# Kernel optimization log

Measured on AMD Instinct MI355X. Metric: run time of the kernel, lower is better.

The kernel has to match this reference:

```python
import jax, jax.numpy as jnp
import numpy as np

N = 100000       # num nodes
E = 1000000      # num edges
D_IN = 128       # input feature dim
D_H = 64         # hidden = output dim
EPS = 1e-5       # GraphNorm eps
SLOPE = 0.2      # LeakyReLU negative slope


def _glorot(key, shape):
    lim = float(np.sqrt(6.0 / (shape[0] + shape[1])))
    return jax.random.uniform(key, shape, jnp.float32, -lim, lim)


def setup_inputs() -> dict:
    key = jax.random.key(0)
    ks = jax.random.split(key, 6)
    return {
        "x": jax.random.normal(ks[0], (N, D_IN), jnp.float32),
        "edge_index": jax.random.randint(ks[1], (2, E), 0, N),
        "W_in": _glorot(ks[2], (D_IN, D_H)),
        "b_in": jnp.zeros((D_H,), jnp.float32),
        "W1": _glorot(ks[3], (D_H, D_H)),
        "b1": jnp.zeros((D_H,), jnp.float32),
        "gn1_alpha": jnp.ones((D_H,), jnp.float32),
        "gn1_gamma": jnp.ones((D_H,), jnp.float32),
        "gn1_beta": jnp.zeros((D_H,), jnp.float32),
        "W2": _glorot(ks[4], (D_H, D_H)),
        "b2": jnp.zeros((D_H,), jnp.float32),
        "gn2_alpha": jnp.ones((D_H,), jnp.float32),
        "gn2_gamma": jnp.ones((D_H,), jnp.float32),
        "gn2_beta": jnp.zeros((D_H,), jnp.float32),
    }


def gcn_conv(x, W, b, src, dst):
    # GCNConv with added self-loops and symmetric normalization:
    # out = D^{-1/2} (A + I) D^{-1/2} (x W) + b
    xw = x @ W                                                 # [N, D]
    ones = jnp.ones((src.shape[0],), x.dtype)
    deg = jax.ops.segment_sum(ones, dst, num_segments=x.shape[0]) + 1.0  # +1 self-loop
    dinv = jax.lax.rsqrt(deg)                                  # [N]
    coef = dinv[src] * dinv[dst]                               # [E]
    agg = jax.ops.segment_sum(xw[src] * coef[:, None], dst, num_segments=x.shape[0])
    return agg + xw * (dinv * dinv)[:, None] + b


def graph_norm(x, alpha, gamma, beta):
    # PyG GraphNorm over a single graph: per-feature mean/var over all nodes
    mean = jnp.mean(x, axis=0)
    c = x - alpha * mean
    var = jnp.mean(c * c, axis=0)
    return gamma * c * jax.lax.rsqrt(var + EPS) + beta


def reference(x, edge_index, W_in, b_in, W1, b1, gn1_alpha, gn1_gamma, gn1_beta,
              W2, b2, gn2_alpha, gn2_gamma, gn2_beta):
    src, dst = edge_index[0], edge_index[1]
    h = x @ W_in + b_in                                        # input projection
    h = graph_norm(gcn_conv(h, W1, b1, src, dst), gn1_alpha, gn1_gamma, gn1_beta)
    h = jnp.where(h > 0, h, SLOPE * h)                         # LeakyReLU(0.2); dropout=eval (identity)
    h = graph_norm(gcn_conv(h, W2, b2, src, dst), gn2_alpha, gn2_gamma, gn2_beta)
    return h                                                    # [N, D_H]
```

## Files before the change

### kernel.cpp

```cpp
#include <hip/hip_runtime.h>
#include <stdint.h>

#define N_NODES 100000
#define N_EDGES 1000000
#define D_IN 128
#define D_H 64
#define EPS 1e-5f
#define SLOPE 0.2f

typedef unsigned short u16;
typedef unsigned int u32;

__device__ __forceinline__ float bf2f(u16 u) {
    union { u32 i; float f; } v; v.i = ((u32)u) << 16; return v.f;
}
__device__ __forceinline__ u16 f2bf(float f) {
    union { float f; u32 i; } v; v.f = f;
    u32 r = (v.i + 0x7fffu + ((v.i >> 16) & 1u)) >> 16;
    return (u16)r;
}
__device__ __forceinline__ bool is_f32(const void* flagp) {
    return *(const u32*)flagp == 0x3F800000u;
}
__device__ __forceinline__ float loadf(const void* p, size_t i, bool m) {
    return m ? ((const float*)p)[i] : bf2f(((const u16*)p)[i]);
}

__global__ void kprep(const void* __restrict__ W_in, const void* __restrict__ b_in,
                      const void* __restrict__ W1, const void* __restrict__ flagp,
                      float* __restrict__ Wc, float* __restrict__ bc)
{
    bool m = is_f32(flagp);
    int c = blockIdx.x;
    int t = threadIdx.x;
    __shared__ float w1c[D_H];
    if (t < D_H) w1c[t] = loadf(W1, t * D_H + c, m);
    __syncthreads();
    float acc = 0.f;
    #pragma unroll 8
    for (int j = 0; j < D_H; j++) acc += loadf(W_in, t * D_H + j, m) * w1c[j];
    Wc[t * D_H + c] = acc;
    if (t == 0) {
        float b = 0.f;
        for (int j = 0; j < D_H; j++) b += loadf(b_in, j, m) * w1c[j];
        bc[c] = b;
    }
}

__global__ void kfill(const int* __restrict__ ei, int* __restrict__ cnt,
                      int* __restrict__ bucket)
{
    int e = blockIdx.x * blockDim.x + threadIdx.x;
    if (e >= N_EDGES) return;
    int s = ei[e];
    int d = ei[N_EDGES + e];
    int slot = atomicAdd(&cnt[d], 1);
    if (slot < 64) bucket[(size_t)d * 64 + slot] = s;
}

__global__ void kdinv(const int* __restrict__ cnt, float* __restrict__ dinv,
                      u16* __restrict__ xwb_pad)
{
    int i = blockIdx.x * blockDim.x + threadIdx.x;
    if (i < D_H) xwb_pad[(size_t)N_NODES * D_H + i] = 0;
    if (i >= N_NODES) return;
    dinv[i] = rsqrtf((float)cnt[i] + 1.0f);
}

__global__ __launch_bounds__(256) void kgemm1(const void* __restrict__ x,
        const float* __restrict__ Wc, const float* __restrict__ bc,
        const float* __restrict__ dinv, const void* __restrict__ flagp,
        u16* __restrict__ xwb)
{
    bool m = is_f32(flagp);
    __shared__ __align__(16) u16 xs[64 * 132];
    __shared__ float WL[D_IN * D_H];
    int tid = threadIdx.x;
    int row0 = blockIdx.x * 64;
    for (int i = tid; i < D_IN * D_H / 4; i += 256)
        ((float4*)WL)[i] = ((const float4*)Wc)[i];
    for (int i = tid; i < 64 * 32; i += 256) {
        int r = i >> 5, kq = (i & 31) * 4;
        int gr = row0 + r;
        ushort4 u = make_ushort4(0, 0, 0, 0);
        if (gr < N_NODES) {
            if (m) {
                float4 v = *(const float4*)((const float*)x + (size_t)gr * D_IN + kq);
                u = make_ushort4(f2bf(v.x), f2bf(v.y), f2bf(v.z), f2bf(v.w));
            } else {
                u = *(const ushort4*)((const u16*)x + (size_t)gr * D_IN + kq);
            }
        }
        *(ushort4*)(xs + r * 132 + kq) = u;
    }
    __syncthreads();
    int tx = tid & 15, ry = tid >> 4;
    float4 bcv = ((const float4*)bc)[tx];
    float acc[4][4];
    #pragma unroll
    for (int j = 0; j < 4; j++) { acc[j][0] = bcv.x; acc[j][1] = bcv.y; acc[j][2] = bcv.z; acc[j][3] = bcv.w; }
    #pragma unroll 4
    for (int k = 0; k < D_IN; k += 2) {
        float4 w0 = *(const float4*)(WL + k * D_H + tx * 4);
        float4 w1 = *(const float4*)(WL + (k + 1) * D_H + tx * 4);
        #pragma unroll
        for (int j = 0; j < 4; j++) {
            u32 p = *(const u32*)(xs + (ry * 4 + j) * 132 + k);
            float xl = bf2f((u16)(p & 0xffffu));
            float xh = bf2f((u16)(p >> 16));
            acc[j][0] += xl * w0.x; acc[j][1] += xl * w0.y; acc[j][2] += xl * w0.z; acc[j][3] += xl * w0.w;
            acc[j][0] += xh * w1.x; acc[j][1] += xh * w1.y; acc[j][2] += xh * w1.z; acc[j][3] += xh * w1.w;
        }
    }
    #pragma unroll
    for (int j = 0; j < 4; j++) {
        int gr = row0 + ry * 4 + j;
        if (gr < N_NODES) {
            float ds = dinv[gr];
            *(ushort4*)(xwb + (size_t)gr * D_H + tx * 4) =
                make_ushort4(f2bf(acc[j][0] * ds), f2bf(acc[j][1] * ds),
                             f2bf(acc[j][2] * ds), f2bf(acc[j][3] * ds));
        }
    }
}

__global__ __launch_bounds__(256) void kagg(const u16* __restrict__ xwb,
        const float* __restrict__ dinv, const int* __restrict__ cnt,
        const int* __restrict__ bucket, const void* __restrict__ bvec,
        const void* __restrict__ flagp, u16* __restrict__ ybuf,
        float* __restrict__ accum)
{
    bool m = is_f32(flagp);
    __shared__ __align__(16) char smem[4][8192];
    __shared__ float red_s[4][64], red_q[4][64];
    int tid = threadIdx.x;
    int wv = tid >> 6, L = tid & 63;
    int half = L >> 5, mm = L & 31;
    int node0 = blockIdx.x * 32 + wv * 8;

    int cnt8 = cnt[node0 + (L & 7)];
    float di8 = dinv[node0 + (L & 7)];
    int deg[8]; float dd[8];
    #pragma unroll
    for (int t = 0; t < 8; t++) {
        deg[t] = min(__builtin_amdgcn_readlane(cnt8, t), 64);
        dd[t] = __uint_as_float(__builtin_amdgcn_readlane(__float_as_uint(di8), t));
    }
    float b0 = loadf(bvec, 2 * mm, m), b1 = loadf(bvec, 2 * mm + 1, m);

    float ls0 = 0, ls1 = 0, lq0 = 0, lq1 = 0;
    char* base = &smem[wv][0];

    #pragma unroll
    for (int b = 0; b < 2; b++) {
        int nb = node0 + b * 4;
        int tl = L >> 4, sl = L & 15;
        int i_l = nb + tl;
        int raw = bucket[(size_t)i_l * 64 + sl];
        int degL = min(__shfl(cnt8, b * 4 + tl), 64);
        int src = (sl < degL) ? raw : ((sl == degL) ? i_l : N_NODES);

        #pragma unroll
        for (int k = 0; k < 8; k++) {
            int srcK = __shfl(src, k * 8 + (L >> 3));
            const u16* gp = xwb + (size_t)srcK * D_H + (L & 7) * 8;
            __builtin_amdgcn_global_load_lds(gp, base + k * 1024, 16, 0, 0);
        }
        __builtin_amdgcn_s_waitcnt(0);
        __builtin_amdgcn_sched_barrier(0);
        asm volatile("" ::: "memory");

        float A0 = 0, A1 = 0, C0 = 0, C1 = 0;
        #pragma unroll
        for (int p = 0; p < 2; p++) {
            int np = p * 2 + half;
            const u32* rp = (const u32*)(base + np * 2048);
            float a0 = 0, a1 = 0;
            #pragma unroll
            for (int s = 0; s < 16; s++) {
                u32 v = rp[s * 32 + mm];
                a0 += __uint_as_float(v << 16);
                a1 += __uint_as_float(v & 0xffff0000u);
            }
            if (p == 0) { A0 = a0; A1 = a1; } else { C0 = a0; C1 = a1; }
        }
        #pragma unroll
        for (int t = 0; t < 4; t++) {
            int degt = deg[b * 4 + t];
            if (degt >= 16) {
                int i = nb + t;
                float r0 = 0, r1 = 0;
                for (int s = 16 + half; s <= degt; s += 2) {
                    int sv = (s < degt) ? bucket[(size_t)i * 64 + s] : i;
                    u32 v = *((const u32*)(xwb + (size_t)sv * D_H) + mm);
                    r0 += __uint_as_float(v << 16);
                    r1 += __uint_as_float(v & 0xffff0000u);
                }
                r0 += __shfl_xor(r0, 32);
                r1 += __shfl_xor(r1, 32);
                bool mine = (half == (t & 1));
                if (t < 2) { A0 += mine ? r0 : 0.f; A1 += mine ? r1 : 0.f; }
                else       { C0 += mine ? r0 : 0.f; C1 += mine ? r1 : 0.f; }
            }
        }
        #pragma unroll
        for (int p = 0; p < 2; p++) {
            float a0 = p ? C0 : A0, a1 = p ? C1 : A1;
            float ddv = half ? dd[b * 4 + p * 2 + 1] : dd[b * 4 + p * 2];
            float y0 = ddv * a0 + b0;
            float y1 = ddv * a1 + b1;
            int node = nb + p * 2 + half;
            ((u32*)(ybuf + (size_t)node * D_H))[mm] =
                (u32)f2bf(y0) | ((u32)f2bf(y1) << 16);
            ls0 += y0; ls1 += y1; lq0 += y0 * y0; lq1 += y1 * y1;
        }
        asm volatile("" ::: "memory");
    }

    ls0 += __shfl_xor(ls0, 32); ls1 += __shfl_xor(ls1, 32);
    lq0 += __shfl_xor(lq0, 32); lq1 += __shfl_xor(lq1, 32);
    if (half == 0) {
        *(float2*)&red_s[wv][2 * mm] = make_float2(ls0, ls1);
        *(float2*)&red_q[wv][2 * mm] = make_float2(lq0, lq1);
    }
    __syncthreads();
    if (tid < 64) {
        atomicAdd(&accum[tid],      red_s[0][tid] + red_s[1][tid] + red_s[2][tid] + red_s[3][tid]);
        atomicAdd(&accum[64 + tid], red_q[0][tid] + red_q[1][tid] + red_q[2][tid] + red_q[3][tid]);
    }
}

__global__ void kparams(const float* __restrict__ accum, const void* __restrict__ alpha,
        const void* __restrict__ gamma, const void* __restrict__ beta,
        const void* __restrict__ flagp, float* __restrict__ params)
{
    bool m = is_f32(flagp);
    int f = threadIdx.x;
    float mean = accum[f] * (1.0f / N_NODES);
    float al = loadf(alpha, f, m);
    float var = accum[64 + f] * (1.0f / N_NODES) - mean * mean * al * (2.0f - al);
    var = fmaxf(var, 0.f);
    float a = loadf(gamma, f, m) * rsqrtf(var + EPS);
    params[f] = a;
    params[64 + f] = loadf(beta, f, m) - a * al * mean;
}

__global__ __launch_bounds__(256) void kgemm2(const u16* __restrict__ y1b,
        const void* __restrict__ W2, const float* __restrict__ params,
        const float* __restrict__ dinv, const void* __restrict__ flagp,
        u16* __restrict__ xwb)
{
    bool m = is_f32(flagp);
    __shared__ __align__(16) u16 hs[64 * 68];
    __shared__ float WL[D_H * D_H];
    __shared__ float aL[64], cL[64];
    int tid = threadIdx.x;
    if (tid < 64) { aL[tid] = params[tid]; cL[tid] = params[64 + tid]; }
    for (int i = tid; i < D_H * D_H; i += 256) WL[i] = loadf(W2, i, m);
    __syncthreads();
    int row0 = blockIdx.x * 64;
    for (int i = tid; i < 64 * 16; i += 256) {
        int r = i >> 4, kq = (i & 15) * 4;
        int gr = row0 + r;
        ushort4 u = make_ushort4(0, 0, 0, 0);
        if (gr < N_NODES) u = *(const ushort4*)(y1b + (size_t)gr * D_H + kq);
        float h0 = aL[kq + 0] * bf2f(u.x) + cL[kq + 0]; h0 = h0 > 0.f ? h0 : SLOPE * h0;
        float h1 = aL[kq + 1] * bf2f(u.y) + cL[kq + 1]; h1 = h1 > 0.f ? h1 : SLOPE * h1;
        float h2 = aL[kq + 2] * bf2f(u.z) + cL[kq + 2]; h2 = h2 > 0.f ? h2 : SLOPE * h2;
        float h3 = aL[kq + 3] * bf2f(u.w) + cL[kq + 3]; h3 = h3 > 0.f ? h3 : SLOPE * h3;
        *(ushort4*)(hs + r * 68 + kq) = make_ushort4(f2bf(h0), f2bf(h1), f2bf(h2), f2bf(h3));
    }
    __syncthreads();
    int tx = tid & 15, ry = tid >> 4;
    float acc[4][4] = {};
    #pragma unroll 4
    for (int k = 0; k < D_H; k += 2) {
        float4 w0 = *(const float4*)(WL + k * D_H + tx * 4);
        float4 w1 = *(const float4*)(WL + (k + 1) * D_H + tx * 4);
        #pragma unroll
        for (int j = 0; j < 4; j++) {
            u32 p = *(const u32*)(hs + (ry * 4 + j) * 68 + k);
            float xl = bf2f((u16)(p & 0xffffu));
            float xh = bf2f((u16)(p >> 16));
            acc[j][0] += xl * w0.x; acc[j][1] += xl * w0.y; acc[j][2] += xl * w0.z; acc[j][3] += xl * w0.w;
            acc[j][0] += xh * w1.x; acc[j][1] += xh * w1.y; acc[j][2] += xh * w1.z; acc[j][3] += xh * w1.w;
        }
    }
    #pragma unroll
    for (int j = 0; j < 4; j++) {
        int gr = row0 + ry * 4 + j;
        if (gr < N_NODES) {
            float ds = dinv[gr];
            *(ushort4*)(xwb + (size_t)gr * D_H + tx * 4) =
                make_ushort4(f2bf(acc[j][0] * ds), f2bf(acc[j][1] * ds),
                             f2bf(acc[j][2] * ds), f2bf(acc[j][3] * ds));
        }
    }
}

__global__ void kout(const u16* __restrict__ y2b, const float* __restrict__ params2,
                     const void* __restrict__ flagp, void* __restrict__ out)
{
    bool m = is_f32(flagp);
    int idx = blockIdx.x * blockDim.x + threadIdx.x;
    if (idx >= N_NODES * D_H) return;
    int f = idx & 63;
    float v = params2[f] * bf2f(y2b[idx]) + params2[64 + f];
    if (m) ((float*)out)[idx] = v;
    else   ((u16*)out)[idx] = f2bf(v);
}

extern "C" void kernel_launch(void* const* d_in, const int* in_sizes, int n_in,
                              void* d_out, int out_size, void* d_ws, size_t ws_size,
                              hipStream_t stream)
{
    const void* x    = d_in[0];
    const int*  ei   = (const int*)d_in[1];
    const void* W_in = d_in[2];
    const void* b_in = d_in[3];
    const void* W1   = d_in[4];
    const void* b1   = d_in[5];
    const void* gn1a = d_in[6];
    const void* gn1g = d_in[7];
    const void* gn1b = d_in[8];
    const void* W2   = d_in[9];
    const void* b2   = d_in[10];
    const void* gn2a = d_in[11];
    const void* gn2g = d_in[12];
    const void* gn2b = d_in[13];

    char* ws = (char*)d_ws;
    int*   cnt    = (int*)(ws + 0);
    float* accum  = (float*)(ws + 400000);
    float* params = (float*)(ws + 401024);
    float* bc     = (float*)(ws + 402048);
    float* Wc     = (float*)(ws + 402432);
    float* dinv   = (float*)(ws + 435200);
    int*   bucket = (int*)(ws + 1235200);
    u16*   bufA   = (u16*)(ws + 26835200);
    u16*   bufB   = (u16*)(ws + 39635456);

    hipMemsetAsync(ws, 0, 400000 + 1024, stream);

    kprep<<<64, 128, 0, stream>>>(W_in, b_in, W1, gn1a, Wc, bc);
    kfill<<<(N_EDGES + 255) / 256, 256, 0, stream>>>(ei, cnt, bucket);
    kdinv<<<(N_NODES + 255) / 256, 256, 0, stream>>>(cnt, dinv, bufA);
    kgemm1<<<(N_NODES + 63) / 64, 256, 0, stream>>>(x, Wc, bc, dinv, gn1a, bufA);
    kagg<<<N_NODES / 32, 256, 0, stream>>>(bufA, dinv, cnt, bucket, b1, gn1a, bufB, accum);
    kparams<<<1, 64, 0, stream>>>(accum, gn1a, gn1g, gn1b, gn1a, params);
    kgemm2<<<(N_NODES + 63) / 64, 256, 0, stream>>>(bufB, W2, params, dinv, gn1a, bufA);
    kagg<<<N_NODES / 32, 256, 0, stream>>>(bufA, dinv, cnt, bucket, b2, gn1a, bufB, accum + 128);
    kparams<<<1, 64, 0, stream>>>(accum + 128, gn2a, gn2g, gn2b, gn1a, params + 128);
    kout<<<(N_NODES * D_H + 255) / 256, 256, 0, stream>>>(bufB, params + 128, gn1a, d_out);
}
```

Before: 434.5 us.

## Use bf16 MFMA instructions for both dense projection GEMMs

Replaces the scalar FP32 FMA inner loops in kgemm1 and kgemm2 with 16x16x32 bf16 MFMA instructions. The combined input weight and W2 are now pre-transposed and stored as bf16 by kprep, so each wave can load its B fragments contiguously from padded LDS. The aim is to cut the ALU cost of the two dense matmuls. In exchange the weights are rounded to bf16, and output stores shrink from ushort4 to scattered 2-byte writes.

```diff
diff --git a/kernel.cpp b/kernel.cpp
--- a/kernel.cpp
+++ b/kernel.cpp
@@ -1,5 +1,6 @@
 #include <hip/hip_runtime.h>
 #include <stdint.h>
+#include <string.h>
 
 #define N_NODES 100000
 #define N_EDGES 1000000
@@ -10,6 +11,8 @@
 
 typedef unsigned short u16;
 typedef unsigned int u32;
+typedef __attribute__((ext_vector_type(8))) short bf16x8;
+typedef __attribute__((ext_vector_type(4))) float f32x4;
 
 __device__ __forceinline__ float bf2f(u16 u) {
     union { u32 i; float f; } v; v.i = ((u32)u) << 16; return v.f;
@@ -27,23 +30,31 @@
 }
 
 __global__ void kprep(const void* __restrict__ W_in, const void* __restrict__ b_in,
-                      const void* __restrict__ W1, const void* __restrict__ flagp,
-                      float* __restrict__ Wc, float* __restrict__ bc)
-{
-    bool m = is_f32(flagp);
-    int c = blockIdx.x;
+                      const void* __restrict__ W1, const void* __restrict__ W2,
+                      const void* __restrict__ flagp,
+                      u16* __restrict__ WcT, u16* __restrict__ W2T,
+                      float* __restrict__ bc)
+{
+    bool m = is_f32(flagp);
     int t = threadIdx.x;
-    __shared__ float w1c[D_H];
-    if (t < D_H) w1c[t] = loadf(W1, t * D_H + c, m);
-    __syncthreads();
-    float acc = 0.f;
-    #pragma unroll 8
-    for (int j = 0; j < D_H; j++) acc += loadf(W_in, t * D_H + j, m) * w1c[j];
-    Wc[t * D_H + c] = acc;
-    if (t == 0) {
-        float b = 0.f;
-        for (int j = 0; j < D_H; j++) b += loadf(b_in, j, m) * w1c[j];
-        bc[c] = b;
+    if (blockIdx.x < 64) {
+        int c = blockIdx.x;
+        __shared__ float w1c[D_H];
+        if (t < D_H) w1c[t] = loadf(W1, t * D_H + c, m);
+        __syncthreads();
+        float acc = 0.f;
+        #pragma unroll 8
+        for (int j = 0; j < D_H; j++) acc += loadf(W_in, t * D_H + j, m) * w1c[j];
+        WcT[c * D_IN + t] = f2bf(acc);
+        if (t == 0) {
+            float b = 0.f;
+            for (int j = 0; j < D_H; j++) b += loadf(b_in, j, m) * w1c[j];
+            bc[c] = b;
+        }
+    } else {
+        int idx = (blockIdx.x - 64) * 128 + t;
+        int n = idx >> 6, k = idx & 63;
+        W2T[n * D_H + k] = f2bf(loadf(W2, k * D_H + n, m));
     }
 }
 
@@ -68,17 +79,19 @@
 }
 
 __global__ __launch_bounds__(256) void kgemm1(const void* __restrict__ x,
-        const float* __restrict__ Wc, const float* __restrict__ bc,
+        const u16* __restrict__ WcT, const float* __restrict__ bc,
         const float* __restrict__ dinv, const void* __restrict__ flagp,
         u16* __restrict__ xwb)
 {
     bool m = is_f32(flagp);
-    __shared__ __align__(16) u16 xs[64 * 132];
-    __shared__ float WL[D_IN * D_H];
+    __shared__ __align__(16) u16 xs[64 * 136];
+    __shared__ __align__(16) u16 WT[64 * 136];
     int tid = threadIdx.x;
     int row0 = blockIdx.x * 64;
-    for (int i = tid; i < D_IN * D_H / 4; i += 256)
-        ((float4*)WL)[i] = ((const float4*)Wc)[i];
+    for (int i = tid; i < 64 * 32; i += 256) {
+        int r = i >> 5, kq = (i & 31) * 4;
+        *(ushort4*)(WT + r * 136 + kq) = *(const ushort4*)(WcT + r * D_IN + kq);
+    }
     for (int i = tid; i < 64 * 32; i += 256) {
         int r = i >> 5, kq = (i & 31) * 4;
         int gr = row0 + r;
@@ -91,35 +104,35 @@
                 u = *(const ushort4*)((const u16*)x + (size_t)gr * D_IN + kq);
             }
         }
-        *(ushort4*)(xs + r * 132 + kq) = u;
+        *(ushort4*)(xs + r * 136 + kq) = u;
     }
     __syncthreads();
-    int tx = tid & 15, ry = tid >> 4;
-    float4 bcv = ((const float4*)bc)[tx];
-    float acc[4][4];
-    #pragma unroll
-    for (int j = 0; j < 4; j++) { acc[j][0] = bcv.x; acc[j][1] = bcv.y; acc[j][2] = bcv.z; acc[j][3] = bcv.w; }
-    #pragma unroll 4
-    for (int k = 0; k < D_IN; k += 2) {
-        float4 w0 = *(const float4*)(WL + k * D_H + tx * 4);
-        float4 w1 = *(const float4*)(WL + (k + 1) * D_H + tx * 4);
-        #pragma unroll
-        for (int j = 0; j < 4; j++) {
-            u32 p = *(const u32*)(xs + (ry * 4 + j) * 132 + k);
-            float xl = bf2f((u16)(p & 0xffffu));
-            float xh = bf2f((u16)(p >> 16));
-            acc[j][0] += xl * w0.x; acc[j][1] += xl * w0.y; acc[j][2] += xl * w0.z; acc[j][3] += xl * w0.w;
-            acc[j][0] += xh * w1.x; acc[j][1] += xh * w1.y; acc[j][2] += xh * w1.z; acc[j][3] += xh * w1.w;
-        }
-    }
-    #pragma unroll
-    for (int j = 0; j < 4; j++) {
-        int gr = row0 + ry * 4 + j;
+    int w = tid >> 6, L = tid & 63;
+    int q = L >> 4, c = L & 15;
+    f32x4 acc[4];
+    #pragma unroll
+    for (int ct = 0; ct < 4; ct++) {
+        float b = bc[ct * 16 + c];
+        acc[ct] = (f32x4){b, b, b, b};
+    }
+    const u16* ap = xs + (w * 16 + c) * 136 + q * 8;
+    #pragma unroll
+    for (int kk = 0; kk < 4; kk++) {
+        bf16x8 af = *(const bf16x8*)(ap + kk * 32);
+        #pragma unroll
+        for (int ct = 0; ct < 4; ct++) {
+            bf16x8 bfr = *(const bf16x8*)(WT + (ct * 16 + c) * 136 + kk * 32 + q * 8);
+            acc[ct] = __builtin_amdgcn_mfma_f32_16x16x32_bf16(af, bfr, acc[ct], 0, 0, 0);
+        }
+    }
+    #pragma unroll
+    for (int r = 0; r < 4; r++) {
+        int gr = row0 + w * 16 + q * 4 + r;
         if (gr < N_NODES) {
             float ds = dinv[gr];
-            *(ushort4*)(xwb + (size_t)gr * D_H + tx * 4) =
-                make_ushort4(f2bf(acc[j][0] * ds), f2bf(acc[j][1] * ds),
-                             f2bf(acc[j][2] * ds), f2bf(acc[j][3] * ds));
+            #pragma unroll
+            for (int ct = 0; ct < 4; ct++)
+                xwb[(size_t)gr * D_H + ct * 16 + c] = f2bf(acc[ct][r] * ds);
         }
     }
 }
@@ -246,17 +259,18 @@
 }
 
 __global__ __launch_bounds__(256) void kgemm2(const u16* __restrict__ y1b,
-        const void* __restrict__ W2, const float* __restrict__ params,
-        const float* __restrict__ dinv, const void* __restrict__ flagp,
-        u16* __restrict__ xwb)
-{
-    bool m = is_f32(flagp);
-    __shared__ __align__(16) u16 hs[64 * 68];
-    __shared__ float WL[D_H * D_H];
+        const u16* __restrict__ W2T, const float* __restrict__ params,
+        const float* __restrict__ dinv, u16* __restrict__ xwb)
+{
+    __shared__ __align__(16) u16 hs[64 * 72];
+    __shared__ __align__(16) u16 WT[64 * 72];
     __shared__ float aL[64], cL[64];
     int tid = threadIdx.x;
     if (tid < 64) { aL[tid] = params[tid]; cL[tid] = params[64 + tid]; }
-    for (int i = tid; i < D_H * D_H; i += 256) WL[i] = loadf(W2, i, m);
+    for (int i = tid; i < 64 * 16; i += 256) {
+        int r = i >> 4, kq = (i & 15) * 4;
+        *(ushort4*)(WT + r * 72 + kq) = *(const ushort4*)(W2T + r * D_H + kq);
+    }
     __syncthreads();
     int row0 = blockIdx.x * 64;
     for (int i = tid; i < 64 * 16; i += 256) {
@@ -268,32 +282,30 @@
         float h1 = aL[kq + 1] * bf2f(u.y) + cL[kq + 1]; h1 = h1 > 0.f ? h1 : SLOPE * h1;
         float h2 = aL[kq + 2] * bf2f(u.z) + cL[kq + 2]; h2 = h2 > 0.f ? h2 : SLOPE * h2;
         float h3 = aL[kq + 3] * bf2f(u.w) + cL[kq + 3]; h3 = h3 > 0.f ? h3 : SLOPE * h3;
-        *(ushort4*)(hs + r * 68 + kq) = make_ushort4(f2bf(h0), f2bf(h1), f2bf(h2), f2bf(h3));
+        *(ushort4*)(hs + r * 72 + kq) = make_ushort4(f2bf(h0), f2bf(h1), f2bf(h2), f2bf(h3));
     }
     __syncthreads();
-    int tx = tid & 15, ry = tid >> 4;
-    float acc[4][4] = {};
-    #pragma unroll 4
-    for (int k = 0; k < D_H; k += 2) {
-        float4 w0 = *(const float4*)(WL + k * D_H + tx * 4);
-        float4 w1 = *(const float4*)(WL + (k + 1) * D_H + tx * 4);
-        #pragma unroll
-        for (int j = 0; j < 4; j++) {
-            u32 p = *(const u32*)(hs + (ry * 4 + j) * 68 + k);
-            float xl = bf2f((u16)(p & 0xffffu));
-            float xh = bf2f((u16)(p >> 16));
-            acc[j][0] += xl * w0.x; acc[j][1] += xl * w0.y; acc[j][2] += xl * w0.z; acc[j][3] += xl * w0.w;
-            acc[j][0] += xh * w1.x; acc[j][1] += xh * w1.y; acc[j][2] += xh * w1.z; acc[j][3] += xh * w1.w;
-        }
-    }
-    #pragma unroll
-    for (int j = 0; j < 4; j++) {
-        int gr = row0 + ry * 4 + j;
+    int w = tid >> 6, L = tid & 63;
+    int q = L >> 4, c = L & 15;
+    f32x4 acc[4] = {};
+    const u16* ap = hs + (w * 16 + c) * 72 + q * 8;
+    #pragma unroll
+    for (int kk = 0; kk < 2; kk++) {
+        bf16x8 af = *(const bf16x8*)(ap + kk * 32);
+        #pragma unroll
+        for (int ct = 0; ct < 4; ct++) {
+            bf16x8 bfr = *(const bf16x8*)(WT + (ct * 16 + c) * 72 + kk * 32 + q * 8);
+            acc[ct] = __builtin_amdgcn_mfma_f32_16x16x32_bf16(af, bfr, acc[ct], 0, 0, 0);
+        }
+    }
+    #pragma unroll
+    for (int r = 0; r < 4; r++) {
+        int gr = row0 + w * 16 + q * 4 + r;
         if (gr < N_NODES) {
             float ds = dinv[gr];
-            *(ushort4*)(xwb + (size_t)gr * D_H + tx * 4) =
-                make_ushort4(f2bf(acc[j][0] * ds), f2bf(acc[j][1] * ds),
-                             f2bf(acc[j][2] * ds), f2bf(acc[j][3] * ds));
+            #pragma unroll
+            for (int ct = 0; ct < 4; ct++)
+                xwb[(size_t)gr * D_H + ct * 16 + c] = f2bf(acc[ct][r] * ds);
         }
     }
 }
@@ -334,7 +346,8 @@
     float* accum  = (float*)(ws + 400000);
     float* params = (float*)(ws + 401024);
     float* bc     = (float*)(ws + 402048);
-    float* Wc     = (float*)(ws + 402432);
+    u16*   WcT    = (u16*)(ws + 402432);
+    u16*   W2T    = (u16*)(ws + 418816);
     float* dinv   = (float*)(ws + 435200);
     int*   bucket = (int*)(ws + 1235200);
     u16*   bufA   = (u16*)(ws + 26835200);
@@ -342,13 +355,13 @@
 
     hipMemsetAsync(ws, 0, 400000 + 1024, stream);
 
-    kprep<<<64, 128, 0, stream>>>(W_in, b_in, W1, gn1a, Wc, bc);
+    kprep<<<96, 128, 0, stream>>>(W_in, b_in, W1, W2, gn1a, WcT, W2T, bc);
     kfill<<<(N_EDGES + 255) / 256, 256, 0, stream>>>(ei, cnt, bucket);
     kdinv<<<(N_NODES + 255) / 256, 256, 0, stream>>>(cnt, dinv, bufA);
-    kgemm1<<<(N_NODES + 63) / 64, 256, 0, stream>>>(x, Wc, bc, dinv, gn1a, bufA);
+    kgemm1<<<(N_NODES + 63) / 64, 256, 0, stream>>>(x, WcT, bc, dinv, gn1a, bufA);
     kagg<<<N_NODES / 32, 256, 0, stream>>>(bufA, dinv, cnt, bucket, b1, gn1a, bufB, accum);
     kparams<<<1, 64, 0, stream>>>(accum, gn1a, gn1g, gn1b, gn1a, params);
-    kgemm2<<<(N_NODES + 63) / 64, 256, 0, stream>>>(bufB, W2, params, dinv, gn1a, bufA);
+    kgemm2<<<(N_NODES + 63) / 64, 256, 0, stream>>>(bufB, W2T, params, dinv, bufA);
     kagg<<<N_NODES / 32, 256, 0, stream>>>(bufA, dinv, cnt, bucket, b2, gn1a, bufB, accum + 128);
     kparams<<<1, 64, 0, stream>>>(accum + 128, gn2a, gn2g, gn2b, gn1a, params + 128);
     kout<<<(N_NODES * D_H + 255) / 256, 256, 0, stream>>>(bufB, params + 128, gn1a, d_out);
```

After: 398.5 us. 1.09x faster.
